# Kernel tuning notes

Measured on AMD Instinct MI355X. Metric: run time of the kernel, lower is better.

## Reference

```python
import jax, jax.numpy as jnp
import numpy as np

EMBED = 768
HEADS = 8
HEAD_DIM = EMBED // HEADS  # 96


def setup_inputs() -> dict:
    key = jax.random.key(0)
    k1, k2, k3, k4, k5 = jax.random.split(key, 5)
    b, n = 4, 2048
    x = jax.random.normal(k1, (b, n, EMBED), dtype=jnp.float32)
    s = 1.0 / np.sqrt(EMBED)
    W_qkv = jax.random.normal(k2, (EMBED, 3 * EMBED), dtype=jnp.float32) * s
    b_qkv = jax.random.normal(k3, (3 * EMBED,), dtype=jnp.float32) * 0.02
    W_proj = jax.random.normal(k4, (EMBED, EMBED), dtype=jnp.float32) * s
    b_proj = jax.random.normal(k5, (EMBED,), dtype=jnp.float32) * 0.02
    return {"x": x, "W_qkv": W_qkv, "b_qkv": b_qkv, "W_proj": W_proj, "b_proj": b_proj}


def reference(x, W_qkv, b_qkv, W_proj, b_proj):
    b, n, _ = x.shape
    qkv = x @ W_qkv + b_qkv  # [b, n, 3*EMBED]
    # rearrange 'b n (h d qkv) -> qkv b h n d': qkv is fastest-varying axis
    qkv = qkv.reshape(b, n, HEADS, HEAD_DIM, 3)
    q = jnp.transpose(qkv[..., 0], (0, 2, 1, 3))  # [b, h, n, d]
    k = jnp.transpose(qkv[..., 1], (0, 2, 1, 3))
    v = jnp.transpose(qkv[..., 2], (0, 2, 1, 3))
    scale = 1.0 / np.sqrt(HEAD_DIM)
    energy = jnp.einsum('bhqd,bhkd->bhqk', q, k) * scale
    attn = jax.nn.softmax(energy, axis=-1)  # dropout p=0 -> identity
    out = jnp.einsum('bhqk,bhkd->bhqd', attn, v)
    out = jnp.transpose(out, (0, 2, 1, 3)).reshape(b, n, EMBED)
    out = out @ W_proj + b_proj
    return out
```

## Files before the change

kernel.cpp:

```cpp
#include <hip/hip_runtime.h>
#include <hip/hip_bf16.h>

#define EMBED 768
#define NHEADS 8
#define HDIM 96
#define SEQ 2048
#define BATCH 4
#define NTOK (BATCH*SEQ)
#define QKVN (3*EMBED)

#define QSCALE 0.14724444f

typedef __attribute__((ext_vector_type(4))) float f32x4;
typedef __attribute__((ext_vector_type(16))) float f32x16;
typedef __attribute__((ext_vector_type(8))) __bf16 bf16x8;

__device__ __forceinline__ unsigned short f2bf(float f) {
  union { float f; unsigned int u; } c; c.f = f;
  unsigned int u = c.u;
  return (unsigned short)((u + 0x7FFFu + ((u >> 16) & 1u)) >> 16);
}

__device__ __forceinline__ unsigned int cvt_pk_bf16(float lo, float hi) {
  unsigned int r;
  asm("v_cvt_pk_bf16_f32 %0, %1, %2" : "=v"(r) : "v"(lo), "v"(hi));
  return r;
}

__device__ __forceinline__ void gload_lds16(const void* g, void* l) {
  __builtin_amdgcn_global_load_lds(
      (const __attribute__((address_space(1))) unsigned int*)g,
      (__attribute__((address_space(3))) unsigned int*)l, 16, 0, 0);
}

__global__ __launch_bounds__(256) void cast_x_kernel(const float4* __restrict__ in,
                                                     ushort4* __restrict__ out, int n4) {
  int i = blockIdx.x * 256 + threadIdx.x;
  if (i >= n4) return;
  float4 v = in[i];
  out[i] = make_ushort4(f2bf(v.x), f2bf(v.y), f2bf(v.z), f2bf(v.w));
}

__global__ __launch_bounds__(256) void transpose_cast_kernel(const float* __restrict__ in,
                                                             unsigned short* __restrict__ out,
                                                             int R, int C, int remap) {
  __shared__ float t[32][33];
  int c0 = blockIdx.x * 32, r0 = blockIdx.y * 32;
  int tx = threadIdx.x & 31, ty = threadIdx.x >> 5;
  #pragma unroll
  for (int i = 0; i < 32; i += 8)
    t[ty + i][tx] = in[(size_t)(r0 + ty + i) * C + c0 + tx];
  __syncthreads();
  #pragma unroll
  for (int i = 0; i < 32; i += 8) {
    int c = c0 + ty + i;
    int rp = remap ? (c % 3) * 768 + c / 3 : c;
    out[(size_t)rp * R + r0 + tx] = f2bf(t[tx][ty + i]);
  }
}

template <int MODE>
__global__ __launch_bounds__(256, 2) void gemm8_kernel(
    const unsigned short* __restrict__ A, const unsigned short* __restrict__ B,
    const float* __restrict__ bias, int K, int NB,
    unsigned short* __restrict__ Qo, unsigned short* __restrict__ Ko,
    unsigned short* __restrict__ Vt, float* __restrict__ out) {
  __shared__ unsigned short As[2][128 * 64];
  __shared__ unsigned short Bs[2][128 * 64];
  const int tid = threadIdx.x;
  const int lane = tid & 63, wid = tid >> 6;
  const int wr = wid >> 1, wc = wid & 1;
  const int l15 = lane & 15, l16 = lane >> 4;
  const int cpx = gridDim.x >> 3;
  const int bid = blockIdx.x;
  const int swz = (bid & 7) * cpx + (bid >> 3);
  const int my = swz / NB, nx = swz - my * NB;
  const int m0 = my * 128, n0 = nx * 128;

  auto stage_half = [&](int buf, int kt, int half) {
    const unsigned short* src = half ? B : A;
    const int base0 = half ? n0 : m0;
    char* dst = (char*)(half ? &Bs[buf][0] : &As[buf][0]);
    #pragma unroll
    for (int i = 0; i < 4; i++) {
      int c = i * 256 + tid;
      int r = c >> 3, s = c & 7;
      gload_lds16(src + (size_t)(base0 + r) * K + kt * 64 + ((s ^ (r & 7)) << 3),
                  dst + (i * 256 + wid * 64) * 16);
    }
  };

  f32x4 acc[4][4] = {};
  const int xr = (l15 & 7) << 4;

  stage_half(0, 0, 0);
  stage_half(0, 0, 1);
  asm volatile("s_waitcnt vmcnt(0)" ::: "memory");
  __builtin_amdgcn_s_barrier();

  const int NT = K >> 6;
  for (int t = 0; t < NT; ++t) {
    const int cur = t & 1;
    const char* Ac = (const char*)&As[cur][0];
    const char* Bc = (const char*)&Bs[cur][0];
    #pragma unroll
    for (int kh = 0; kh < 2; ++kh) {
      bf16x8 af[4], bfr[4];
      #pragma unroll
      for (int mi = 0; mi < 4; mi++)
        af[mi] = *(const bf16x8*)(Ac + (wr * 64 + mi * 16 + l15) * 128 +
                                  ((kh * 64 + l16 * 16) ^ xr));
      #pragma unroll
      for (int ni = 0; ni < 4; ni++)
        bfr[ni] = *(const bf16x8*)(Bc + (wc * 64 + ni * 16 + l15) * 128 +
                                   ((kh * 64 + l16 * 16) ^ xr));
      if (t + 1 < NT) stage_half(cur ^ 1, t + 1, kh);
      __builtin_amdgcn_s_barrier();
      __builtin_amdgcn_s_setprio(1);
      #pragma unroll
      for (int mi = 0; mi < 4; mi++)
        #pragma unroll
        for (int ni = 0; ni < 4; ni++)
          acc[mi][ni] = __builtin_amdgcn_mfma_f32_16x16x32_bf16(af[mi], bfr[ni], acc[mi][ni], 0, 0, 0);
      __builtin_amdgcn_s_setprio(0);
      __builtin_amdgcn_s_barrier();
    }
    asm volatile("s_waitcnt lgkmcnt(0)" ::: "memory");
    asm volatile("s_waitcnt vmcnt(0)" ::: "memory");
    __builtin_amdgcn_sched_barrier(0);
    __builtin_amdgcn_s_barrier();
  }

  if (MODE == 0) {
    #pragma unroll
    for (int mi = 0; mi < 4; mi++) {
      #pragma unroll
      for (int ni = 0; ni < 4; ni++) {
        int base = n0 + wc * 64 + ni * 16;
        int which = base / 768;
        int hd = base - which * 768;
        int h = hd / 96;
        int d0 = hd - h * 96;
        float bb = bias[(hd + l15) * 3 + which];
        int rowb = m0 + wr * 64 + mi * 16 + l16 * 4;
        int bi = rowb >> 11, nnb = rowb & 2047;
        size_t bh = (size_t)(bi * NHEADS + h);
        if (which == 2) {
          int nn2 = (nnb & ~12) | ((nnb & 4) << 1) | ((nnb & 8) >> 1);
          float v0 = acc[mi][ni][0] + bb, v1 = acc[mi][ni][1] + bb;
          float v2 = acc[mi][ni][2] + bb, v3 = acc[mi][ni][3] + bb;
          uint2 pk;
          pk.x = cvt_pk_bf16(v0, v1);
          pk.y = cvt_pk_bf16(v2, v3);
          *(uint2*)(Vt + (bh * HDIM + d0 + l15) * SEQ + nn2) = pk;
        } else {
          #pragma unroll
          for (int j = 0; j < 4; j++) {
            float v = acc[mi][ni][j] + bb;
            int nn = nnb + j;
            if (which == 0) Qo[(bh * SEQ + nn) * HDIM + d0 + l15] = f2bf(v * QSCALE);
            else            Ko[(bh * SEQ + nn) * HDIM + d0 + l15] = f2bf(v);
          }
        }
      }
    }
  } else {
    #pragma unroll
    for (int mi = 0; mi < 4; mi++) {
      #pragma unroll
      for (int ni = 0; ni < 4; ni++) {
        int col = n0 + wc * 64 + ni * 16 + l15;
        float bb = bias[col];
        #pragma unroll
        for (int j = 0; j < 4; j++) {
          int row = m0 + wr * 64 + mi * 16 + l16 * 4 + j;
          out[(size_t)row * EMBED + col] = acc[mi][ni][j] + bb;
        }
      }
    }
  }
}

__global__ __launch_bounds__(256) void attn_kernel(
    const unsigned short* __restrict__ Q, const unsigned short* __restrict__ Kd,
    const unsigned short* __restrict__ Vt, unsigned short* __restrict__ Oa) {
  __shared__ unsigned short Ks[2][64 * 96];
  __shared__ unsigned short Vs[2][96 * 64];

  const int tid = threadIdx.x, lane = tid & 63, wid = tid >> 6;
  const int l31 = lane & 31, hi = lane >> 5;
  const int bid = blockIdx.x;
  const int swz = (bid & 7) * 64 + (bid >> 3);
  const int qb_ = swz & 15, bh = swz >> 4;
  const int bi = bh >> 3, h = bh & 7;
  const int q0 = qb_ * 128;

  const unsigned short* Qg = Q + ((size_t)bh * SEQ + q0) * HDIM;
  const unsigned short* Kg = Kd + (size_t)bh * SEQ * HDIM;
  const unsigned short* Vg = Vt + (size_t)bh * HDIM * SEQ;

  bf16x8 qf[6];
  #pragma unroll
  for (int ks = 0; ks < 6; ks++)
    qf[ks] = *(const bf16x8*)(Qg + (size_t)(wid * 32 + l31) * HDIM + ks * 16 + hi * 8);

  auto stageKV = [&](int buf, int k0) {
    #pragma unroll
    for (int i = 0; i < 3; i++) {
      int g = i * 256 + tid;
      int o = g >> 6, kv = g & 63;
      gload_lds16(Kg + (size_t)(k0 + kv) * HDIM + o * 8,
                  (char*)&Ks[buf][0] + (i * 256 + wid * 64) * 16);
    }
    #pragma unroll
    for (int i = 0; i < 3; i++) {
      int idx = i * 256 + tid;
      int d = idx >> 3, s = idx & 7;
      gload_lds16(Vg + (size_t)d * SEQ + k0 + ((s ^ (d & 7)) << 3),
                  (char*)&Vs[buf][0] + (i * 256 + wid * 64) * 16);
    }
  };

  f32x16 oacc[3] = {};
  float mrow = -__builtin_inff(), lrow = 0.f;

  stageKV(0, 0);
  __syncthreads();

  for (int kb = 0; kb < SEQ / 64; kb++) {
    const int cur = kb & 1;
    if (kb + 1 < SEQ / 64) stageKV(cur ^ 1, (kb + 1) * 64);

    const char* Kc = (const char*)&Ks[cur][0];
    const char* Vc = (const char*)&Vs[cur][0];

    f32x16 sacc[2] = {};
    #pragma unroll
    for (int ks = 0; ks < 6; ks++) {
      bf16x8 ak0 = *(const bf16x8*)(Kc + (((2 * ks + hi) * 64) + l31) * 16);
      bf16x8 ak1 = *(const bf16x8*)(Kc + (((2 * ks + hi) * 64) + 32 + l31) * 16);
      __builtin_amdgcn_s_setprio(1);
      sacc[0] = __builtin_amdgcn_mfma_f32_32x32x16_bf16(ak0, qf[ks], sacc[0], 0, 0, 0);
      sacc[1] = __builtin_amdgcn_mfma_f32_32x32x16_bf16(ak1, qf[ks], sacc[1], 0, 0, 0);
      __builtin_amdgcn_s_setprio(0);
    }

    float v = fmaxf(sacc[0][0], sacc[1][0]);
    #pragma unroll
    for (int r = 1; r < 16; r++)
      v = fmaxf(v, fmaxf(sacc[0][r], sacc[1][r]));
    v = fmaxf(v, __shfl_xor(v, 32));
    if (!__all(v - mrow <= 11.54f)) {
      float mnew = fmaxf(mrow, v);
      float alpha = __builtin_amdgcn_exp2f(mrow - mnew);
      mrow = mnew;
      lrow *= alpha;
      #pragma unroll
      for (int db = 0; db < 3; db++)
        #pragma unroll
        for (int r = 0; r < 16; r++)
          oacc[db][r] *= alpha;
    }

    unsigned int pk[2][8];
    float psum = 0.f;
    #pragma unroll
    for (int kbk = 0; kbk < 2; kbk++)
      #pragma unroll
      for (int j2 = 0; j2 < 8; j2++) {
        float p0 = __builtin_amdgcn_exp2f(sacc[kbk][2 * j2] - mrow);
        float p1 = __builtin_amdgcn_exp2f(sacc[kbk][2 * j2 + 1] - mrow);
        psum += p0 + p1;
        pk[kbk][j2] = cvt_pk_bf16(p0, p1);
      }
    psum += __shfl_xor(psum, 32);
    lrow += psum;

    #pragma unroll
    for (int kbk = 0; kbk < 2; kbk++)
      #pragma unroll
      for (int t = 0; t < 2; t++) {
        union { unsigned int u[4]; bf16x8 v; } pf;
        pf.u[0] = pk[kbk][4 * t];     pf.u[1] = pk[kbk][4 * t + 1];
        pf.u[2] = pk[kbk][4 * t + 2]; pf.u[3] = pk[kbk][4 * t + 3];
        const int sidx = (kbk * 2 + t) * 2 + hi;
        __builtin_amdgcn_s_setprio(1);
        #pragma unroll
        for (int db = 0; db < 3; db++) {
          int d = db * 32 + l31;
          bf16x8 vb = *(const bf16x8*)(Vc + d * 128 + ((sidx ^ (d & 7)) << 4));
          oacc[db] = __builtin_amdgcn_mfma_f32_32x32x16_bf16(vb, pf.v, oacc[db], 0, 0, 0);
        }
        __builtin_amdgcn_s_setprio(0);
      }

    __syncthreads();
  }

  {
    const float rl = 1.f / lrow;
    const int tok = q0 + wid * 32 + l31;
    unsigned short* Og = Oa + ((size_t)bi * SEQ + tok) * EMBED + h * HDIM;
    #pragma unroll
    for (int db = 0; db < 3; db++)
      #pragma unroll
      for (int rq = 0; rq < 4; rq++) {
        uint2 o;
        o.x = cvt_pk_bf16(oacc[db][4 * rq] * rl, oacc[db][4 * rq + 1] * rl);
        o.y = cvt_pk_bf16(oacc[db][4 * rq + 2] * rl, oacc[db][4 * rq + 3] * rl);
        *(uint2*)(Og + db * 32 + rq * 8 + hi * 4) = o;
      }
  }
}

extern "C" void kernel_launch(void* const* d_in, const int* in_sizes, int n_in,
                              void* d_out, int out_size, void* d_ws, size_t ws_size,
                              hipStream_t stream) {
  const float* x      = (const float*)d_in[0];
  const float* W_qkv  = (const float*)d_in[1];
  const float* b_qkv  = (const float*)d_in[2];
  const float* W_proj = (const float*)d_in[3];
  const float* b_proj = (const float*)d_in[4];
  float* out = (float*)d_out;

  char* ws = (char*)d_ws;
  size_t off = 0;
  auto alloc = [&](size_t bytes) { void* p = ws + off; off += (bytes + 255) & ~(size_t)255; return p; };
  unsigned short* xb  = (unsigned short*)alloc((size_t)NTOK * EMBED * 2);
  unsigned short* WqT = (unsigned short*)alloc((size_t)QKVN * EMBED * 2);
  unsigned short* WpT = (unsigned short*)alloc((size_t)EMBED * EMBED * 2);
  unsigned short* Qb  = (unsigned short*)alloc((size_t)NTOK * EMBED * 2);
  unsigned short* Kb  = (unsigned short*)alloc((size_t)NTOK * EMBED * 2);
  unsigned short* Vtb = (unsigned short*)alloc((size_t)NTOK * EMBED * 2);
  unsigned short* Ob  = (unsigned short*)alloc((size_t)NTOK * EMBED * 2);

  cast_x_kernel<<<dim3(NTOK * EMBED / 4 / 256), dim3(256), 0, stream>>>(
      (const float4*)x, (ushort4*)xb, NTOK * EMBED / 4);
  transpose_cast_kernel<<<dim3(QKVN / 32, EMBED / 32), dim3(256), 0, stream>>>(W_qkv, WqT, EMBED, QKVN, 1);
  transpose_cast_kernel<<<dim3(EMBED / 32, EMBED / 32), dim3(256), 0, stream>>>(W_proj, WpT, EMBED, EMBED, 0);

  gemm8_kernel<0><<<dim3((NTOK / 128) * (QKVN / 128)), dim3(256), 0, stream>>>(
      xb, WqT, b_qkv, EMBED, QKVN / 128, Qb, Kb, Vtb, nullptr);

  attn_kernel<<<dim3(BATCH * NHEADS * (SEQ / 128)), dim3(256), 0, stream>>>(Qb, Kb, Vtb, Ob);

  gemm8_kernel<1><<<dim3((NTOK / 128) * (EMBED / 128)), dim3(256), 0, stream>>>(
      Ob, WpT, b_proj, EMBED, EMBED / 128, nullptr, nullptr, nullptr, out);
}
```

Baseline: 158.1 us.

## Split attention over KV halves with separate merge kernel

Each query tile now processes only half of the keys, doubling the attention grid, with KV tiles reduced from 64 to 32 rows and smaller LDS buffers. Partial normalized outputs and per-row max/sum statistics are written out, and a new merge kernel combines the two halves with log-sum-exp weights into the head-interleaved layout. This aims to raise occupancy and CU utilization, at the cost of extra global traffic, an additional launch, more frequent per-tile syncs and reductions, and bf16 rounding of the partials.

```diff
diff --git a/kernel.cpp b/kernel.cpp
--- a/kernel.cpp
+++ b/kernel.cpp
@@ -8,6 +8,7 @@
 #define BATCH 4
 #define NTOK (BATCH*SEQ)
 #define QKVN (3*EMBED)
+#define NROW (32*SEQ)
 
 #define QSCALE 0.14724444f
 
@@ -183,17 +184,21 @@
 
 __global__ __launch_bounds__(256) void attn_kernel(
     const unsigned short* __restrict__ Q, const unsigned short* __restrict__ Kd,
-    const unsigned short* __restrict__ Vt, unsigned short* __restrict__ Oa) {
-  __shared__ unsigned short Ks[2][64 * 96];
-  __shared__ unsigned short Vs[2][96 * 64];
+    const unsigned short* __restrict__ Vt,
+    unsigned short* __restrict__ Op0, unsigned short* __restrict__ Op1,
+    float2* __restrict__ ml) {
+  __shared__ unsigned short Ks[2][32 * 96];
+  __shared__ unsigned short Vs[2][96 * 32];
 
   const int tid = threadIdx.x, lane = tid & 63, wid = tid >> 6;
   const int l31 = lane & 31, hi = lane >> 5;
   const int bid = blockIdx.x;
-  const int swz = (bid & 7) * 64 + (bid >> 3);
-  const int qb_ = swz & 15, bh = swz >> 4;
-  const int bi = bh >> 3, h = bh & 7;
-  const int q0 = qb_ * 128;
+  const int swz = (bid & 7) * 128 + (bid >> 3);
+  const int bh = swz >> 5;
+  const int qt = (swz >> 1) & 15;
+  const int split = swz & 1;
+  const int q0 = qt * 128;
+  const int kvbase = split * (SEQ / 2);
 
   const unsigned short* Qg = Q + ((size_t)bh * SEQ + q0) * HDIM;
   const unsigned short* Kg = Kd + (size_t)bh * SEQ * HDIM;
@@ -207,48 +212,46 @@
   auto stageKV = [&](int buf, int k0) {
     #pragma unroll
     for (int i = 0; i < 3; i++) {
-      int g = i * 256 + tid;
-      int o = g >> 6, kv = g & 63;
-      gload_lds16(Kg + (size_t)(k0 + kv) * HDIM + o * 8,
-                  (char*)&Ks[buf][0] + (i * 256 + wid * 64) * 16);
-    }
-    #pragma unroll
-    for (int i = 0; i < 3; i++) {
       int idx = i * 256 + tid;
-      int d = idx >> 3, s = idx & 7;
-      gload_lds16(Vg + (size_t)d * SEQ + k0 + ((s ^ (d & 7)) << 3),
-                  (char*)&Vs[buf][0] + (i * 256 + wid * 64) * 16);
+      if (idx < 384) {
+        int o = idx >> 5, kv = idx & 31;
+        gload_lds16(Kg + (size_t)(k0 + kv) * HDIM + o * 8,
+                    (char*)&Ks[buf][0] + idx * 16);
+      } else {
+        int j = idx - 384;
+        int d = j >> 2, s = j & 3;
+        gload_lds16(Vg + (size_t)d * SEQ + k0 + ((s ^ ((d >> 1) & 3)) << 3),
+                    (char*)&Vs[buf][0] + j * 16);
+      }
     }
   };
 
   f32x16 oacc[3] = {};
   float mrow = -__builtin_inff(), lrow = 0.f;
 
-  stageKV(0, 0);
+  stageKV(0, kvbase);
   __syncthreads();
 
-  for (int kb = 0; kb < SEQ / 64; kb++) {
+  const int NI = (SEQ / 2) / 32;
+  for (int kb = 0; kb < NI; kb++) {
     const int cur = kb & 1;
-    if (kb + 1 < SEQ / 64) stageKV(cur ^ 1, (kb + 1) * 64);
+    if (kb + 1 < NI) stageKV(cur ^ 1, kvbase + (kb + 1) * 32);
 
     const char* Kc = (const char*)&Ks[cur][0];
     const char* Vc = (const char*)&Vs[cur][0];
 
-    f32x16 sacc[2] = {};
+    f32x16 sacc = {};
     #pragma unroll
     for (int ks = 0; ks < 6; ks++) {
-      bf16x8 ak0 = *(const bf16x8*)(Kc + (((2 * ks + hi) * 64) + l31) * 16);
-      bf16x8 ak1 = *(const bf16x8*)(Kc + (((2 * ks + hi) * 64) + 32 + l31) * 16);
+      bf16x8 ak = *(const bf16x8*)(Kc + (((2 * ks + hi) * 32) + l31) * 16);
       __builtin_amdgcn_s_setprio(1);
-      sacc[0] = __builtin_amdgcn_mfma_f32_32x32x16_bf16(ak0, qf[ks], sacc[0], 0, 0, 0);
-      sacc[1] = __builtin_amdgcn_mfma_f32_32x32x16_bf16(ak1, qf[ks], sacc[1], 0, 0, 0);
+      sacc = __builtin_amdgcn_mfma_f32_32x32x16_bf16(ak, qf[ks], sacc, 0, 0, 0);
       __builtin_amdgcn_s_setprio(0);
     }
 
-    float v = fmaxf(sacc[0][0], sacc[1][0]);
-    #pragma unroll
-    for (int r = 1; r < 16; r++)
-      v = fmaxf(v, fmaxf(sacc[0][r], sacc[1][r]));
+    float v = fmaxf(sacc[0], sacc[1]);
+    #pragma unroll
+    for (int r = 2; r < 16; r++) v = fmaxf(v, sacc[r]);
     v = fmaxf(v, __shfl_xor(v, 32));
     if (!__all(v - mrow <= 11.54f)) {
       float mnew = fmaxf(mrow, v);
@@ -262,45 +265,41 @@
           oacc[db][r] *= alpha;
     }
 
-    unsigned int pk[2][8];
+    unsigned int pk[8];
     float psum = 0.f;
     #pragma unroll
-    for (int kbk = 0; kbk < 2; kbk++)
-      #pragma unroll
-      for (int j2 = 0; j2 < 8; j2++) {
-        float p0 = __builtin_amdgcn_exp2f(sacc[kbk][2 * j2] - mrow);
-        float p1 = __builtin_amdgcn_exp2f(sacc[kbk][2 * j2 + 1] - mrow);
-        psum += p0 + p1;
-        pk[kbk][j2] = cvt_pk_bf16(p0, p1);
-      }
+    for (int j2 = 0; j2 < 8; j2++) {
+      float p0 = __builtin_amdgcn_exp2f(sacc[2 * j2] - mrow);
+      float p1 = __builtin_amdgcn_exp2f(sacc[2 * j2 + 1] - mrow);
+      psum += p0 + p1;
+      pk[j2] = cvt_pk_bf16(p0, p1);
+    }
     psum += __shfl_xor(psum, 32);
     lrow += psum;
 
     #pragma unroll
-    for (int kbk = 0; kbk < 2; kbk++)
-      #pragma unroll
-      for (int t = 0; t < 2; t++) {
-        union { unsigned int u[4]; bf16x8 v; } pf;
-        pf.u[0] = pk[kbk][4 * t];     pf.u[1] = pk[kbk][4 * t + 1];
-        pf.u[2] = pk[kbk][4 * t + 2]; pf.u[3] = pk[kbk][4 * t + 3];
-        const int sidx = (kbk * 2 + t) * 2 + hi;
-        __builtin_amdgcn_s_setprio(1);
-        #pragma unroll
-        for (int db = 0; db < 3; db++) {
-          int d = db * 32 + l31;
-          bf16x8 vb = *(const bf16x8*)(Vc + d * 128 + ((sidx ^ (d & 7)) << 4));
-          oacc[db] = __builtin_amdgcn_mfma_f32_32x32x16_bf16(vb, pf.v, oacc[db], 0, 0, 0);
-        }
-        __builtin_amdgcn_s_setprio(0);
-      }
+    for (int tt = 0; tt < 2; tt++) {
+      union { unsigned int u[4]; bf16x8 v; } pf;
+      pf.u[0] = pk[4 * tt];     pf.u[1] = pk[4 * tt + 1];
+      pf.u[2] = pk[4 * tt + 2]; pf.u[3] = pk[4 * tt + 3];
+      const int sidx = tt * 2 + hi;
+      __builtin_amdgcn_s_setprio(1);
+      #pragma unroll
+      for (int db = 0; db < 3; db++) {
+        int d = db * 32 + l31;
+        bf16x8 vb = *(const bf16x8*)(Vc + d * 64 + ((sidx ^ ((d >> 1) & 3)) << 4));
+        oacc[db] = __builtin_amdgcn_mfma_f32_32x32x16_bf16(vb, pf.v, oacc[db], 0, 0, 0);
+      }
+      __builtin_amdgcn_s_setprio(0);
+    }
 
     __syncthreads();
   }
 
   {
     const float rl = 1.f / lrow;
-    const int tok = q0 + wid * 32 + l31;
-    unsigned short* Og = Oa + ((size_t)bi * SEQ + tok) * EMBED + h * HDIM;
+    const int rowq = bh * SEQ + q0 + wid * 32 + l31;
+    unsigned short* Od = (split ? Op1 : Op0) + (size_t)rowq * HDIM;
     #pragma unroll
     for (int db = 0; db < 3; db++)
       #pragma unroll
@@ -308,9 +307,42 @@
         uint2 o;
         o.x = cvt_pk_bf16(oacc[db][4 * rq] * rl, oacc[db][4 * rq + 1] * rl);
         o.y = cvt_pk_bf16(oacc[db][4 * rq + 2] * rl, oacc[db][4 * rq + 3] * rl);
-        *(uint2*)(Og + db * 32 + rq * 8 + hi * 4) = o;
-      }
-  }
+        *(uint2*)(Od + db * 32 + rq * 8 + hi * 4) = o;
+      }
+    if (hi == 0) ml[(size_t)split * NROW + rowq] = make_float2(mrow, lrow);
+  }
+}
+
+__global__ __launch_bounds__(256) void merge_kernel(
+    const unsigned short* __restrict__ Op0, const unsigned short* __restrict__ Op1,
+    const float2* __restrict__ ml, unsigned short* __restrict__ Oa) {
+  int idx = blockIdx.x * 256 + threadIdx.x;
+  int oct = idx % 12, row = idx / 12;
+  float2 a = ml[row], b = ml[NROW + row];
+  float m = fmaxf(a.x, b.x);
+  float w1 = a.y * __builtin_amdgcn_exp2f(a.x - m);
+  float w2 = b.y * __builtin_amdgcn_exp2f(b.x - m);
+  float rs = 1.f / (w1 + w2);
+  w1 *= rs; w2 *= rs;
+  bf16x8 o1 = *(const bf16x8*)(Op0 + (size_t)row * HDIM + oct * 8);
+  bf16x8 o2 = *(const bf16x8*)(Op1 + (size_t)row * HDIM + oct * 8);
+  int bh = row >> 11, q = row & 2047;
+  int bi = bh >> 3, h = bh & 7;
+  unsigned short* dst = Oa + ((size_t)bi * SEQ + q) * EMBED + h * HDIM + oct * 8;
+  uint4 o;
+  float f0 = (float)o1[0] * w1 + (float)o2[0] * w2;
+  float f1 = (float)o1[1] * w1 + (float)o2[1] * w2;
+  float f2 = (float)o1[2] * w1 + (float)o2[2] * w2;
+  float f3 = (float)o1[3] * w1 + (float)o2[3] * w2;
+  float f4 = (float)o1[4] * w1 + (float)o2[4] * w2;
+  float f5 = (float)o1[5] * w1 + (float)o2[5] * w2;
+  float f6 = (float)o1[6] * w1 + (float)o2[6] * w2;
+  float f7 = (float)o1[7] * w1 + (float)o2[7] * w2;
+  o.x = cvt_pk_bf16(f0, f1);
+  o.y = cvt_pk_bf16(f2, f3);
+  o.z = cvt_pk_bf16(f4, f5);
+  o.w = cvt_pk_bf16(f6, f7);
+  *(uint4*)dst = o;
 }
 
 extern "C" void kernel_launch(void* const* d_in, const int* in_sizes, int n_in,
@@ -333,6 +365,9 @@
   unsigned short* Kb  = (unsigned short*)alloc((size_t)NTOK * EMBED * 2);
   unsigned short* Vtb = (unsigned short*)alloc((size_t)NTOK * EMBED * 2);
   unsigned short* Ob  = (unsigned short*)alloc((size_t)NTOK * EMBED * 2);
+  unsigned short* Op1 = (unsigned short*)alloc((size_t)NROW * HDIM * 2);
+  float2*         mlb = (float2*)alloc((size_t)2 * NROW * sizeof(float2));
+  unsigned short* Op0 = xb;
 
   cast_x_kernel<<<dim3(NTOK * EMBED / 4 / 256), dim3(256), 0, stream>>>(
       (const float4*)x, (ushort4*)xb, NTOK * EMBED / 4);
@@ -342,7 +377,8 @@
   gemm8_kernel<0><<<dim3((NTOK / 128) * (QKVN / 128)), dim3(256), 0, stream>>>(
       xb, WqT, b_qkv, EMBED, QKVN / 128, Qb, Kb, Vtb, nullptr);
 
-  attn_kernel<<<dim3(BATCH * NHEADS * (SEQ / 128)), dim3(256), 0, stream>>>(Qb, Kb, Vtb, Ob);
+  attn_kernel<<<dim3(1024), dim3(256), 0, stream>>>(Qb, Kb, Vtb, Op0, Op1, mlb);
+  merge_kernel<<<dim3(NROW * 12 / 256), dim3(256), 0, stream>>>(Op0, Op1, mlb, Ob);
 
   gemm8_kernel<1><<<dim3((NTOK / 128) * (EMBED / 128)), dim3(256), 0, stream>>>(
       Ob, WpT, b_proj, EMBED, EMBED / 128, nullptr, nullptr, nullptr, out);
```

Result: slower. 176.1 us (+11.4%).

## Shrink attention blocks to 64 queries and single-buffer K/V tiles

Applied to the files above, without the earlier changes.

The attention kernel drops from 256 threads handling 128 queries per block to 128 threads handling 64 queries, launching twice as many blocks with a remapped block swizzle. The double-buffered K/V shared-memory staging is replaced by a single buffer that is loaded and then synchronized before compute on each iteration. This halves per-block LDS use so more blocks can reside per CU, aiming at higher occupancy and better latency hiding across blocks. In exchange, global-to-LDS loads no longer overlap compute within a block, and each K/V tile is fetched by twice as many blocks, raising L2 and memory traffic.

```diff
diff --git a/kernel.cpp b/kernel.cpp
--- a/kernel.cpp
+++ b/kernel.cpp
@@ -181,19 +181,20 @@
   }
 }
 
-__global__ __launch_bounds__(256) void attn_kernel(
+__global__ __launch_bounds__(128) void attn_kernel(
     const unsigned short* __restrict__ Q, const unsigned short* __restrict__ Kd,
     const unsigned short* __restrict__ Vt, unsigned short* __restrict__ Oa) {
-  __shared__ unsigned short Ks[2][64 * 96];
-  __shared__ unsigned short Vs[2][96 * 64];
+  __shared__ unsigned short Ks[64 * 96];
+  __shared__ unsigned short Vs[96 * 64];
 
   const int tid = threadIdx.x, lane = tid & 63, wid = tid >> 6;
   const int l31 = lane & 31, hi = lane >> 5;
   const int bid = blockIdx.x;
-  const int swz = (bid & 7) * 64 + (bid >> 3);
-  const int qb_ = swz & 15, bh = swz >> 4;
+  const int swz = (bid & 7) * 128 + (bid >> 3);
+  const int bh = swz >> 5;
+  const int qt = swz & 31;
   const int bi = bh >> 3, h = bh & 7;
-  const int q0 = qb_ * 128;
+  const int q0 = qt * 64;
 
   const unsigned short* Qg = Q + ((size_t)bh * SEQ + q0) * HDIM;
   const unsigned short* Kg = Kd + (size_t)bh * SEQ * HDIM;
@@ -204,35 +205,33 @@
   for (int ks = 0; ks < 6; ks++)
     qf[ks] = *(const bf16x8*)(Qg + (size_t)(wid * 32 + l31) * HDIM + ks * 16 + hi * 8);
 
-  auto stageKV = [&](int buf, int k0) {
-    #pragma unroll
-    for (int i = 0; i < 3; i++) {
-      int g = i * 256 + tid;
+  auto stageKV = [&](int k0) {
+    #pragma unroll
+    for (int i = 0; i < 6; i++) {
+      int g = i * 128 + tid;
       int o = g >> 6, kv = g & 63;
       gload_lds16(Kg + (size_t)(k0 + kv) * HDIM + o * 8,
-                  (char*)&Ks[buf][0] + (i * 256 + wid * 64) * 16);
-    }
-    #pragma unroll
-    for (int i = 0; i < 3; i++) {
-      int idx = i * 256 + tid;
+                  (char*)Ks + (i * 128 + wid * 64) * 16);
+    }
+    #pragma unroll
+    for (int i = 0; i < 6; i++) {
+      int idx = i * 128 + tid;
       int d = idx >> 3, s = idx & 7;
       gload_lds16(Vg + (size_t)d * SEQ + k0 + ((s ^ (d & 7)) << 3),
-                  (char*)&Vs[buf][0] + (i * 256 + wid * 64) * 16);
+                  (char*)Vs + (i * 128 + wid * 64) * 16);
     }
   };
 
   f32x16 oacc[3] = {};
   float mrow = -__builtin_inff(), lrow = 0.f;
 
-  stageKV(0, 0);
-  __syncthreads();
-
-  for (int kb = 0; kb < SEQ / 64; kb++) {
-    const int cur = kb & 1;
-    if (kb + 1 < SEQ / 64) stageKV(cur ^ 1, (kb + 1) * 64);
-
-    const char* Kc = (const char*)&Ks[cur][0];
-    const char* Vc = (const char*)&Vs[cur][0];
+  const int NT = SEQ / 64;
+  for (int kb = 0; kb < NT; kb++) {
+    stageKV(kb * 64);
+    __syncthreads();
+
+    const char* Kc = (const char*)Ks;
+    const char* Vc = (const char*)Vs;
 
     f32x16 sacc[2] = {};
     #pragma unroll
@@ -279,11 +278,11 @@
     #pragma unroll
     for (int kbk = 0; kbk < 2; kbk++)
       #pragma unroll
-      for (int t = 0; t < 2; t++) {
+      for (int tt = 0; tt < 2; tt++) {
         union { unsigned int u[4]; bf16x8 v; } pf;
-        pf.u[0] = pk[kbk][4 * t];     pf.u[1] = pk[kbk][4 * t + 1];
-        pf.u[2] = pk[kbk][4 * t + 2]; pf.u[3] = pk[kbk][4 * t + 3];
-        const int sidx = (kbk * 2 + t) * 2 + hi;
+        pf.u[0] = pk[kbk][4 * tt];     pf.u[1] = pk[kbk][4 * tt + 1];
+        pf.u[2] = pk[kbk][4 * tt + 2]; pf.u[3] = pk[kbk][4 * tt + 3];
+        const int sidx = (kbk * 2 + tt) * 2 + hi;
         __builtin_amdgcn_s_setprio(1);
         #pragma unroll
         for (int db = 0; db < 3; db++) {
@@ -342,7 +341,7 @@
   gemm8_kernel<0><<<dim3((NTOK / 128) * (QKVN / 128)), dim3(256), 0, stream>>>(
       xb, WqT, b_qkv, EMBED, QKVN / 128, Qb, Kb, Vtb, nullptr);
 
-  attn_kernel<<<dim3(BATCH * NHEADS * (SEQ / 128)), dim3(256), 0, stream>>>(Qb, Kb, Vtb, Ob);
+  attn_kernel<<<dim3(1024), dim3(128), 0, stream>>>(Qb, Kb, Vtb, Ob);
 
   gemm8_kernel<1><<<dim3((NTOK / 128) * (EMBED / 128)), dim3(256), 0, stream>>>(
       Ob, WpT, b_proj, EMBED, EMBED / 128, nullptr, nullptr, nullptr, out);
```

Measured after the change: 172.2 us. 8.9% more time.
